# Kernel tuning notes

Hardware: AMD Instinct MI355X
Metric: run time of the kernel (lower is better)

The kernel has to match this reference:

```python
import jax, jax.numpy as jnp
import numpy as np

B, S, D, H, NL, V = 2, 512, 768, 12, 6, 32000
HD = D // H
EPS = 1e-6
# Faithful to original buffer: tril(ones, diagonal=-1) -> True strictly below diagonal,
# and masked_fill sets those to -inf (so each query attends to keys k >= q, as in the source).
MASK = jnp.tril(jnp.ones((S, S), dtype=bool), k=-1)


def setup_inputs() -> dict:
    key = jax.random.key(0)
    ks = jax.random.split(key, 12)
    sc = 0.02
    n = lambda k, shp: jax.random.normal(k, shp, dtype=jnp.float32) * sc
    return {
        "x": jax.random.randint(ks[0], (B, S), 0, V),
        "token_emb": n(ks[1], (V, D)),
        "pos_emb": n(ks[2], (S, D)),
        "norm1_s": jnp.ones((NL, D)), "norm1_b": jnp.zeros((NL, D)),
        "norm2_s": jnp.ones((NL, D)), "norm2_b": jnp.zeros((NL, D)),
        "wq": n(ks[3], (NL, D, D)), "wk": n(ks[4], (NL, D, D)), "wv": n(ks[5], (NL, D, D)),
        "wo": n(ks[6], (NL, D, D)), "bo": jnp.zeros((NL, D)),
        "w1": n(ks[7], (NL, D, 4 * D)), "b1": jnp.zeros((NL, 4 * D)),
        "w2": n(ks[8], (NL, 4 * D, D)), "b2": jnp.zeros((NL, D)),
        "final_s": jnp.ones((D,)), "final_b": jnp.zeros((D,)),
        "head_w": n(ks[9], (D, V)), "head_b": jnp.zeros((V,)),
    }


def _norm(x, s, b):
    # DummyNorm: torch.std default is unbiased (ddof=1); divides by (std + eps), no sqrt(var+eps)
    mean = x.mean(axis=-1, keepdims=True)
    std = jnp.std(x, axis=-1, ddof=1, keepdims=True)
    return s * (x - mean) / (std + EPS) + b


def _gelu(x):
    return 0.5 * x * (1.0 + jnp.tanh(jnp.sqrt(2.0 / jnp.pi) * (x + 0.044715 * x ** 3)))


def _block(x, p):
    wq, wk, wv, wo, bo, w1, b1, w2, b2, n1s, n1b, n2s, n2b = p
    res = x
    h = _norm(x, n1s, n1b)
    q = jnp.einsum("bsd,de->bse", h, wq).reshape(B, S, H, HD)
    k = jnp.einsum("bsd,de->bse", h, wk).reshape(B, S, H, HD)
    v = jnp.einsum("bsd,de->bse", h, wv).reshape(B, S, H, HD)
    scores = jnp.einsum("bqhd,bkhd->bhqk", q, k)
    scores = jnp.where(MASK, -jnp.inf, scores)
    w = jax.nn.softmax(scores / jnp.float32(HD) ** 0.5, axis=-1)  # dropout: eval mode (identity)
    ctx = jnp.einsum("bhqk,bkhd->bqhd", w, v).reshape(B, S, D)
    x = res + (ctx @ wo + bo)
    res = x
    h = _norm(x, n2s, n2b)
    x = res + (_gelu(h @ w1 + b1) @ w2 + b2)
    return x


def reference(x, token_emb, pos_emb, norm1_s, norm1_b, norm2_s, norm2_b,
              wq, wk, wv, wo, bo, w1, b1, w2, b2, final_s, final_b, head_w, head_b):
    h = token_emb[x] + pos_emb[None, :S, :]  # dropout is identity in eval
    params = (wq, wk, wv, wo, bo, w1, b1, w2, b2, norm1_s, norm1_b, norm2_s, norm2_b)
    h = jax.lax.scan(lambda c, p: (_block(c, p), None), h, params)[0]
    h = _norm(h, final_s, final_b)
    return h @ head_w + head_b  # [B, S, V]
```

## Files before the change

kernel.cpp:

```cpp
#include <hip/hip_runtime.h>
#include <math.h>

#define BDIM 2
#define SEQ 512
#define DMODEL 768
#define NHEAD 12
#define HDIM 64
#define NLAYER 6
#define VOCAB 32000
#define MROWS (BDIM*SEQ)
#define EPSV 1e-6f

typedef unsigned short u16;
typedef unsigned int u32;
typedef __bf16 bf16x8 __attribute__((ext_vector_type(8)));
typedef float f32x4 __attribute__((ext_vector_type(4)));

__device__ __forceinline__ u16 f2bf(float f) {
    union { float f; u32 u; } v; v.f = f;
    u32 r = v.u + 0x7fffu + ((v.u >> 16) & 1u);
    return (u16)(r >> 16);
}
__device__ __forceinline__ float bf2f(u16 b) {
    union { u32 u; float f; } v; v.u = ((u32)b) << 16;
    return v.f;
}

__device__ __forceinline__ void gload16(const u16* g, u16* l) {
    __builtin_amdgcn_global_load_lds(
        (const __attribute__((address_space(1))) unsigned int*)g,
        (__attribute__((address_space(3))) unsigned int*)l,
        16, 0, 0);
}

__global__ void embed_kernel(const int* __restrict__ x, const float* __restrict__ tok,
                             const float* __restrict__ pos, float* __restrict__ h) {
    int i = blockIdx.x * blockDim.x + threadIdx.x;
    if (i >= MROWS * DMODEL) return;
    int bs = i / DMODEL, d = i - bs * DMODEL;
    int s = bs & (SEQ - 1);
    h[i] = tok[(size_t)x[bs] * DMODEL + d] + pos[(size_t)s * DMODEL + d];
}

__global__ __launch_bounds__(256) void transpose_conv(const float* __restrict__ in, u16* __restrict__ out,
                                                      int K, int N, long in_bs, long out_bs) {
    __shared__ float t[64][65];
    int b = blockIdx.z;
    int n0 = blockIdx.x * 64, k0 = blockIdx.y * 64;
    int tid = threadIdx.x;
    const float* ip = in + (size_t)b * in_bs;
    int kr = tid >> 4, nc = (tid & 15) * 4;
    #pragma unroll
    for (int i = 0; i < 4; ++i) {
        float4 v = *(const float4*)(ip + (size_t)(k0 + kr + i * 16) * N + n0 + nc);
        t[kr + i * 16][nc] = v.x; t[kr + i * 16][nc + 1] = v.y;
        t[kr + i * 16][nc + 2] = v.z; t[kr + i * 16][nc + 3] = v.w;
    }
    __syncthreads();
    u16* op = out + (size_t)b * out_bs;
    int nr = tid >> 4, kc = (tid & 15) * 4;
    #pragma unroll
    for (int i = 0; i < 4; ++i) {
        ushort4 s;
        s.x = f2bf(t[kc + 0][nr + i * 16]);
        s.y = f2bf(t[kc + 1][nr + i * 16]);
        s.z = f2bf(t[kc + 2][nr + i * 16]);
        s.w = f2bf(t[kc + 3][nr + i * 16]);
        *(ushort4*)(op + (size_t)(n0 + nr + i * 16) * K + k0 + kc) = s;
    }
}

template<bool OUTBF>
__global__ __launch_bounds__(256) void norm_kernel(const float* __restrict__ in,
                                                   const float* __restrict__ scale,
                                                   const float* __restrict__ bias,
                                                   void* __restrict__ outp) {
    int row = blockIdx.x;
    const float* xr = in + (size_t)row * DMODEL;
    int t = threadIdx.x;
    float v0 = xr[t], v1 = xr[t + 256], v2 = xr[t + 512];

    float s = v0 + v1 + v2;
    for (int o = 32; o > 0; o >>= 1) s += __shfl_down(s, o);
    __shared__ float red1[4];
    __shared__ float red2[4];
    int wid = t >> 6, lane = t & 63;
    if (lane == 0) red1[wid] = s;
    __syncthreads();
    float mean = (red1[0] + red1[1] + red1[2] + red1[3]) * (1.0f / DMODEL);

    float d0 = v0 - mean, d1 = v1 - mean, d2 = v2 - mean;
    float ss = d0 * d0 + d1 * d1 + d2 * d2;
    for (int o = 32; o > 0; o >>= 1) ss += __shfl_xor(ss, o);
    if (lane == 0) red2[wid] = ss;
    __syncthreads();
    float var = (red2[0] + red2[1] + red2[2] + red2[3]) * (1.0f / (DMODEL - 1));
    float inv = 1.0f / (sqrtf(var) + EPSV);

    size_t o0 = (size_t)row * DMODEL + t;
    float r0 = scale[t] * d0 * inv + bias[t];
    float r1 = scale[t + 256] * d1 * inv + bias[t + 256];
    float r2 = scale[t + 512] * d2 * inv + bias[t + 512];
    if (OUTBF) {
        u16* out = (u16*)outp;
        out[o0] = f2bf(r0); out[o0 + 256] = f2bf(r1); out[o0 + 512] = f2bf(r2);
    } else {
        float* out = (float*)outp;
        out[o0] = r0; out[o0 + 256] = r1; out[o0 + 512] = r2;
    }
}


template<bool OUTBF, bool BIAS, bool RES, bool GELU, bool SWZ>
__global__ __launch_bounds__(256) void gemm_bf16(const u16* __restrict__ A,
                                                 const u16* __restrict__ Wt,
                                                 const float* __restrict__ bias,
                                                 const float* __restrict__ res,
                                                 void* __restrict__ Cout,
                                                 int M, int N, int K) {
    __shared__ u16 Alds[2][128 * 64];
    __shared__ u16 Blds[2][128 * 64];
    int tid = threadIdx.x;
    int lane = tid & 63;
    int wid = tid >> 6;
    int l15 = lane & 15, lk = lane >> 4;
    int wm = (wid >> 1) * 64, wn = (wid & 1) * 64;
    int bm, bn;
    if (SWZ) {
        int id = blockIdx.x;
        int xcd = id & 7, j = id >> 3;
        int g = xcd * ((int)gridDim.x >> 3) + j;
        int mb = M >> 7;
        bn = (g / mb) * 128;
        bm = (g % mb) * 128;
    } else {
        bm = blockIdx.y * 128; bn = blockIdx.x * 128;
    }

    f32x4 acc[4][4];
    #pragma unroll
    for (int i = 0; i < 4; ++i)
        #pragma unroll
        for (int j = 0; j < 4; ++j) { f32x4 z = {0.f, 0.f, 0.f, 0.f}; acc[i][j] = z; }

    int lr  = lane >> 3;
    int lc8 = (lane & 7) ^ lr;
    const u16* gA = A  + (size_t)(bm + lr) * K + lc8 * 8;
    const u16* gB = Wt + (size_t)(bn + lr) * K + lc8 * 8;
    int wrow = wid * 32;

    auto STAGE = [&](int buf, int k0) {
        #pragma unroll
        for (int i = 0; i < 4; ++i) {
            int rb = wrow + i * 8;
            gload16(gA + (size_t)rb * K + k0, &Alds[buf][rb * 64]);
            gload16(gB + (size_t)rb * K + k0, &Blds[buf][rb * 64]);
        }
    };

    STAGE(0, 0);
    __syncthreads();
    int nt = K >> 6;
    int cur = 0;
    for (int t = 0; t < nt; ++t) {
        if (t + 1 < nt) STAGE(cur ^ 1, (t + 1) << 6);

        #pragma unroll
        for (int s = 0; s < 2; ++s) {
            bf16x8 af[4], bfv[4];
            #pragma unroll
            for (int mi = 0; mi < 4; ++mi) {
                int R = wm + mi * 16 + l15;
                af[mi] = *(const bf16x8*)&Alds[cur][R * 64 + (((s * 4 + lk) ^ (R & 7)) << 3)];
            }
            #pragma unroll
            for (int ni = 0; ni < 4; ++ni) {
                int R = wn + ni * 16 + l15;
                bfv[ni] = *(const bf16x8*)&Blds[cur][R * 64 + (((s * 4 + lk) ^ (R & 7)) << 3)];
            }
            #pragma unroll
            for (int mi = 0; mi < 4; ++mi)
                #pragma unroll
                for (int ni = 0; ni < 4; ++ni)
                    acc[mi][ni] = __builtin_amdgcn_mfma_f32_16x16x32_bf16(af[mi], bfv[ni], acc[mi][ni], 0, 0, 0);
        }
        __syncthreads();
        cur ^= 1;
    }

    #pragma unroll
    for (int mi = 0; mi < 4; ++mi) {
        int row0 = bm + wm + mi * 16 + lk * 4;
        #pragma unroll
        for (int ni = 0; ni < 4; ++ni) {
            int col = bn + wn + ni * 16 + l15;
            float bv = BIAS ? bias[col] : 0.0f;
            #pragma unroll
            for (int rr = 0; rr < 4; ++rr) {
                int row = row0 + rr;
                float v = acc[mi][ni][rr] + bv;
                if (GELU) {
                    float xg = v;
                    v = 0.5f * xg * (1.0f + tanhf(0.7978845608028654f * (xg + 0.044715f * xg * xg * xg)));
                }
                if (RES) v += res[(size_t)row * N + col];
                if (OUTBF) ((u16*)Cout)[(size_t)row * N + col] = f2bf(v);
                else       ((float*)Cout)[(size_t)row * N + col] = v;
            }
        }
    }
}

template<bool OUTBF, bool BIAS, bool RES, bool GELU, int BM, int BN>
__global__ __launch_bounds__(256) void gemm_sm(const u16* __restrict__ A,
                                               const u16* __restrict__ Wt,
                                               const float* __restrict__ bias,
                                               const float* __restrict__ res,
                                               void* __restrict__ Cout,
                                               int M, int N, int K) {
    __shared__ u16 Alds[2][BM * 64];
    __shared__ u16 Blds[2][BN * 64];
    int tid = threadIdx.x;
    int lane = tid & 63;
    int wid = tid >> 6;
    int l15 = lane & 15, lk = lane >> 4;
    int wr = wid >> 1, wc = wid & 1;
    int id = blockIdx.x;
    int xcd = id & 7, j = id >> 3;
    int g = xcd * ((int)gridDim.x >> 3) + j;
    int mb = M / BM;
    int bn = (g / mb) * BN;
    int bm = (g % mb) * BM;
    constexpr int MI = BM / 32;
    constexpr int NI = BN / 32;

    f32x4 acc[MI][NI];
    #pragma unroll
    for (int i = 0; i < MI; ++i)
        #pragma unroll
        for (int j2 = 0; j2 < NI; ++j2) { f32x4 z = {0.f, 0.f, 0.f, 0.f}; acc[i][j2] = z; }

    int lr  = lane >> 3;
    int lc8 = (lane & 7) ^ lr;
    const u16* gA = A  + (size_t)(bm + lr) * K + lc8 * 8;
    const u16* gB = Wt + (size_t)(bn + lr) * K + lc8 * 8;

    auto STAGE = [&](int buf, int k0) {
        #pragma unroll
        for (int i = 0; i < MI; ++i) {
            int rb = wid * (BM / 4) + i * 8;
            gload16(gA + (size_t)rb * K + k0, &Alds[buf][rb * 64]);
        }
        #pragma unroll
        for (int i = 0; i < NI; ++i) {
            int rb = wid * (BN / 4) + i * 8;
            gload16(gB + (size_t)rb * K + k0, &Blds[buf][rb * 64]);
        }
    };

    STAGE(0, 0);
    __syncthreads();
    int nt = K >> 6;
    int cur = 0;
    for (int t = 0; t < nt; ++t) {
        if (t + 1 < nt) STAGE(cur ^ 1, (t + 1) << 6);

        #pragma unroll
        for (int s = 0; s < 2; ++s) {
            bf16x8 af[MI], bfv[NI];
            #pragma unroll
            for (int mi = 0; mi < MI; ++mi) {
                int R = wr * (BM / 2) + mi * 16 + l15;
                af[mi] = *(const bf16x8*)&Alds[cur][R * 64 + (((s * 4 + lk) ^ (R & 7)) << 3)];
            }
            #pragma unroll
            for (int ni = 0; ni < NI; ++ni) {
                int R = wc * (BN / 2) + ni * 16 + l15;
                bfv[ni] = *(const bf16x8*)&Blds[cur][R * 64 + (((s * 4 + lk) ^ (R & 7)) << 3)];
            }
            #pragma unroll
            for (int mi = 0; mi < MI; ++mi)
                #pragma unroll
                for (int ni = 0; ni < NI; ++ni)
                    acc[mi][ni] = __builtin_amdgcn_mfma_f32_16x16x32_bf16(af[mi], bfv[ni], acc[mi][ni], 0, 0, 0);
        }
        __syncthreads();
        cur ^= 1;
    }

    #pragma unroll
    for (int mi = 0; mi < MI; ++mi) {
        int row0 = bm + wr * (BM / 2) + mi * 16 + lk * 4;
        #pragma unroll
        for (int ni = 0; ni < NI; ++ni) {
            int col = bn + wc * (BN / 2) + ni * 16 + l15;
            float bv = BIAS ? bias[col] : 0.0f;
            #pragma unroll
            for (int rr = 0; rr < 4; ++rr) {
                int row = row0 + rr;
                float v = acc[mi][ni][rr] + bv;
                if (GELU) {
                    float xg = v;
                    v = 0.5f * xg * (1.0f + tanhf(0.7978845608028654f * (xg + 0.044715f * xg * xg * xg)));
                }
                if (RES) v += res[(size_t)row * N + col];
                if (OUTBF) ((u16*)Cout)[(size_t)row * N + col] = f2bf(v);
                else       ((float*)Cout)[(size_t)row * N + col] = v;
            }
        }
    }
}

__device__ __forceinline__ float bcast_q(float f0, float f1, float f2, float f3, int l15) {
    int src = (l15 >> 2) * 16;
    float a = __shfl(f0, src, 64);
    float b = __shfl(f1, src, 64);
    float c = __shfl(f2, src, 64);
    float d = __shfl(f3, src, 64);
    int r = l15 & 3;
    return r == 0 ? a : (r == 1 ? b : (r == 2 ? c : d));
}

__global__ __launch_bounds__(256) void attn_mfma(const u16* __restrict__ qkv, u16* __restrict__ ctx) {
    int id = blockIdx.x;
    int slot = id & 7, r0_ = id >> 3;
    int qt = r0_ & 7;
    int bh = (r0_ >> 3) * 8 + slot;
    int b = bh / NHEAD, h = bh % NHEAD;
    int tid = threadIdx.x;
    int w = tid >> 6, lane = tid & 63;
    int l15 = lane & 15, lk = lane >> 4;

    __shared__ u16 Klds[64][72];
    __shared__ u16 Vt[64][72];
    __shared__ u16 Plds[4][16][72];

    int q0 = qt * 64;
    const u16* qbase = qkv + (size_t)(b * SEQ + q0 + w * 16 + l15) * 2304 + h * HDIM;
    bf16x8 qf0 = *(const bf16x8*)(qbase + lk * 8);
    bf16x8 qf1 = *(const bf16x8*)(qbase + 32 + lk * 8);

    f32x4 acc_o[4];
    #pragma unroll
    for (int i = 0; i < 4; ++i) { f32x4 z = {0.f,0.f,0.f,0.f}; acc_o[i] = z; }
    float m_run[4] = {-INFINITY, -INFINITY, -INFINITY, -INFINITY};
    float l_run[4] = {0.f, 0.f, 0.f, 0.f};

    int srow = tid >> 2, sc = (tid & 3) * 16;
    int vcol = srow ^ ((sc >> 4) << 4);
    const u16* kg = qkv + (size_t)(b * SEQ) * 2304 + 768  + h * HDIM;
    const u16* vg = qkv + (size_t)(b * SEQ) * 2304 + 1536 + h * HDIM;

    for (int kt = qt; kt < SEQ / 64; ++kt) {
        int kk0 = kt * 64;
        const u16* kp = kg + (size_t)(kk0 + srow) * 2304 + sc;
        const u16* vp = vg + (size_t)(kk0 + srow) * 2304 + sc;
        uint4 kv0 = *(const uint4*)kp, kv1 = *(const uint4*)(kp + 8);
        uint4 vv0 = *(const uint4*)vp, vv1 = *(const uint4*)(vp + 8);
        __syncthreads();
        *(uint4*)&Klds[srow][sc]     = kv0;
        *(uint4*)&Klds[srow][sc + 8] = kv1;
        {
            const u16* vs = (const u16*)&vv0;
            #pragma unroll
            for (int i = 0; i < 8; ++i) Vt[sc + i][vcol] = vs[i];
            const u16* vs1 = (const u16*)&vv1;
            #pragma unroll
            for (int i = 0; i < 8; ++i) Vt[sc + 8 + i][vcol] = vs1[i];
        }
        __syncthreads();

        f32x4 accs[4];
        #pragma unroll
        for (int kb = 0; kb < 4; ++kb) { f32x4 z = {0.f,0.f,0.f,0.f}; accs[kb] = z; }
        __builtin_amdgcn_s_setprio(1);
        #pragma unroll
        for (int kb = 0; kb < 4; ++kb) {
            bf16x8 kf0 = *(const bf16x8*)&Klds[kb * 16 + l15][lk * 8];
            bf16x8 kf1 = *(const bf16x8*)&Klds[kb * 16 + l15][32 + lk * 8];
            accs[kb] = __builtin_amdgcn_mfma_f32_16x16x32_bf16(qf0, kf0, accs[kb], 0, 0, 0);
            accs[kb] = __builtin_amdgcn_mfma_f32_16x16x32_bf16(qf1, kf1, accs[kb], 0, 0, 0);
        }
        __builtin_amdgcn_s_setprio(0);

        bool diag = (kt == qt);
        float s[4][4];
        #pragma unroll
        for (int kb = 0; kb < 4; ++kb)
            #pragma unroll
            for (int r = 0; r < 4; ++r) {
                float v = accs[kb][r] * 0.125f;
                if (diag && (kk0 + kb * 16 + l15) < (q0 + w * 16 + lk * 4 + r)) v = -INFINITY;
                s[kb][r] = v;
            }
        float fac[4];
        #pragma unroll
        for (int r = 0; r < 4; ++r) {
            float mx = fmaxf(fmaxf(s[0][r], s[1][r]), fmaxf(s[2][r], s[3][r]));
            #pragma unroll
            for (int o = 8; o >= 1; o >>= 1) mx = fmaxf(mx, __shfl_xor(mx, o, 64));
            float mn = fmaxf(m_run[r], mx);
            fac[r] = expf(m_run[r] - mn);
            m_run[r] = mn;
        }
        u16 pb[4][4];
        #pragma unroll
        for (int r = 0; r < 4; ++r) {
            float rs = 0.f;
            #pragma unroll
            for (int kb = 0; kb < 4; ++kb) {
                float p = expf(s[kb][r] - m_run[r]);
                pb[kb][r] = f2bf(p);
                rs += p;
            }
            #pragma unroll
            for (int o = 8; o >= 1; o >>= 1) rs += __shfl_xor(rs, o, 64);
            l_run[r] = l_run[r] * fac[r] + rs;
        }
        #pragma unroll
        for (int kb = 0; kb < 4; ++kb)
            #pragma unroll
            for (int r = 0; r < 4; ++r)
                Plds[w][lk * 4 + r][kb * 16 + l15] = pb[kb][r];
        float fq = bcast_q(fac[0], fac[1], fac[2], fac[3], l15);
        #pragma unroll
        for (int db = 0; db < 4; ++db)
            #pragma unroll
            for (int r = 0; r < 4; ++r) acc_o[db][r] *= fq;
        __syncthreads();

        __builtin_amdgcn_s_setprio(1);
        #pragma unroll
        for (int ks = 0; ks < 2; ++ks) {
            bf16x8 pf = *(const bf16x8*)&Plds[w][l15][ks * 32 + lk * 8];
            #pragma unroll
            for (int db = 0; db < 4; ++db) {
                bf16x8 vf = *(const bf16x8*)&Vt[db * 16 + l15][(ks * 32 + lk * 8) ^ (db << 4)];
                acc_o[db] = __builtin_amdgcn_mfma_f32_16x16x32_bf16(vf, pf, acc_o[db], 0, 0, 0);
            }
        }
        __builtin_amdgcn_s_setprio(0);
    }

    float invq;
    {
        float i0 = 1.0f / l_run[0], i1 = 1.0f / l_run[1], i2 = 1.0f / l_run[2], i3 = 1.0f / l_run[3];
        invq = bcast_q(i0, i1, i2, i3, l15);
    }
    u16* cp = ctx + (size_t)(b * SEQ + q0 + w * 16 + l15) * DMODEL + h * HDIM;
    #pragma unroll
    for (int db = 0; db < 4; ++db) {
        ushort4 st;
        st.x = f2bf(acc_o[db][0] * invq);
        st.y = f2bf(acc_o[db][1] * invq);
        st.z = f2bf(acc_o[db][2] * invq);
        st.w = f2bf(acc_o[db][3] * invq);
        *(ushort4*)(cp + db * 16 + lk * 4) = st;
    }
}

template<bool BIAS, bool RES, bool GELU>
__global__ __launch_bounds__(256) void gemm_f32(const float* __restrict__ A, const float* __restrict__ W,
                                                const float* __restrict__ bias, const float* __restrict__ res,
                                                float* __restrict__ C, int M, int N, int K) {
    const int BM = 64, BN = 64, BK = 16;
    __shared__ float sA[BK][BM + 4];
    __shared__ float sB[BK][BN + 4];
    int tid = threadIdx.x;
    int tx = tid & 15, ty = tid >> 4;
    int bm = blockIdx.y * BM, bn = blockIdx.x * BN;
    float acc[4][4] = {};
    const float* Ab = A + (size_t)bm * K;
    const float* Wb = W + bn;
    for (int k0 = 0; k0 < K; k0 += BK) {
        {
            int rr = tid >> 2, c = (tid & 3) * 4;
            float4 va = *(const float4*)(Ab + (size_t)rr * K + k0 + c);
            sA[c + 0][rr] = va.x; sA[c + 1][rr] = va.y; sA[c + 2][rr] = va.z; sA[c + 3][rr] = va.w;
        }
        {
            int rr = tid >> 4, c = (tid & 15) * 4;
            float4 vb = *(const float4*)(Wb + (size_t)(k0 + rr) * N + c);
            *(float4*)(&sB[rr][c]) = vb;
        }
        __syncthreads();
        #pragma unroll
        for (int kk = 0; kk < BK; ++kk) {
            float4 a4 = *(const float4*)(&sA[kk][ty * 4]);
            float4 b4 = *(const float4*)(&sB[kk][tx * 4]);
            float a[4] = {a4.x, a4.y, a4.z, a4.w};
            float b[4] = {b4.x, b4.y, b4.z, b4.w};
            #pragma unroll
            for (int i = 0; i < 4; ++i)
                #pragma unroll
                for (int j = 0; j < 4; ++j) acc[i][j] += a[i] * b[j];
        }
        __syncthreads();
    }
    #pragma unroll
    for (int i = 0; i < 4; ++i) {
        int row = bm + ty * 4 + i;
        #pragma unroll
        for (int j = 0; j < 4; ++j) {
            int col = bn + tx * 4 + j;
            float v = acc[i][j];
            if (BIAS) v += bias[col];
            if (GELU) { float xg = v; v = 0.5f * xg * (1.0f + tanhf(0.7978845608028654f * (xg + 0.044715f * xg * xg * xg))); }
            if (RES) v += res[(size_t)row * N + col];
            C[(size_t)row * N + col] = v;
        }
    }
}

__global__ __launch_bounds__(256) void attn_f32(const float* __restrict__ q, const float* __restrict__ k,
                                                const float* __restrict__ v, float* __restrict__ ctx) {
    int blk = blockIdx.x;
    int qi = blk & (SEQ - 1);
    int tmp = blk >> 9;
    int h = tmp % NHEAD;
    int b = tmp / NHEAD;
    int tid = threadIdx.x;
    __shared__ float qv[HDIM];
    __shared__ float p[SEQ];
    __shared__ float rmax[4];
    __shared__ float rsum[4];
    __shared__ float part[4][HDIM];
    const float* qptr = q + ((size_t)(b * SEQ + qi) * DMODEL + h * HDIM);
    if (tid < HDIM) qv[tid] = qptr[tid];
    __syncthreads();
    float sc[2];
    #pragma unroll
    for (int c = 0; c < 2; ++c) {
        int kk = tid + c * 256;
        const float* kptr = k + ((size_t)(b * SEQ + kk) * DMODEL + h * HDIM);
        float dot = 0.0f;
        #pragma unroll
        for (int d = 0; d < HDIM; ++d) dot += qv[d] * kptr[d];
        sc[c] = (kk >= qi) ? dot * 0.125f : -INFINITY;
    }
    int wid = tid >> 6, lane = tid & 63;
    float m = fmaxf(sc[0], sc[1]);
    for (int o = 32; o > 0; o >>= 1) m = fmaxf(m, __shfl_down(m, o));
    if (lane == 0) rmax[wid] = m;
    __syncthreads();
    m = fmaxf(fmaxf(rmax[0], rmax[1]), fmaxf(rmax[2], rmax[3]));
    float e0 = expf(sc[0] - m);
    float e1 = expf(sc[1] - m);
    p[tid] = e0; p[tid + 256] = e1;
    float sum = e0 + e1;
    for (int o = 32; o > 0; o >>= 1) sum += __shfl_down(sum, o);
    if (lane == 0) rsum[wid] = sum;
    __syncthreads();
    float inv = 1.0f / (rsum[0] + rsum[1] + rsum[2] + rsum[3]);
    int d = tid & 63, ch = tid >> 6;
    float accv = 0.0f;
    const float* vbase = v + ((size_t)b * SEQ * DMODEL + h * HDIM + d);
    for (int kk = ch * 128; kk < (ch + 1) * 128; ++kk) accv += p[kk] * vbase[(size_t)kk * DMODEL];
    part[ch][d] = accv;
    __syncthreads();
    if (tid < HDIM) {
        float rv = (part[0][tid] + part[1][tid] + part[2][tid] + part[3][tid]) * inv;
        ctx[((size_t)(b * SEQ + qi) * DMODEL + h * HDIM + tid)] = rv;
    }
}

extern "C" void kernel_launch(void* const* d_in, const int* in_sizes, int n_in,
                              void* d_out, int out_size, void* d_ws, size_t ws_size,
                              hipStream_t stream) {
    const int*   x   = (const int*)d_in[0];
    const float* tok = (const float*)d_in[1];
    const float* pos = (const float*)d_in[2];
    const float* n1s = (const float*)d_in[3];
    const float* n1b = (const float*)d_in[4];
    const float* n2s = (const float*)d_in[5];
    const float* n2b = (const float*)d_in[6];
    const float* wq  = (const float*)d_in[7];
    const float* wk  = (const float*)d_in[8];
    const float* wv  = (const float*)d_in[9];
    const float* wo  = (const float*)d_in[10];
    const float* bo  = (const float*)d_in[11];
    const float* w1  = (const float*)d_in[12];
    const float* b1  = (const float*)d_in[13];
    const float* w2  = (const float*)d_in[14];
    const float* b2  = (const float*)d_in[15];
    const float* fs  = (const float*)d_in[16];
    const float* fb  = (const float*)d_in[17];
    const float* hw  = (const float*)d_in[18];
    const float* hb  = (const float*)d_in[19];
    float* out = (float*)d_out;

    const size_t szWtQKV = (size_t)NLAYER * 2304 * 768 * 2;
    const size_t szWtO   = (size_t)NLAYER * 768 * 768 * 2;
    const size_t szWt1   = (size_t)NLAYER * 3072 * 768 * 2;
    const size_t szWt2   = (size_t)NLAYER * 768 * 3072 * 2;
    const size_t szWtH   = (size_t)VOCAB * 768 * 2;
    const size_t szH     = (size_t)MROWS * DMODEL * 4;
    const size_t szHN    = (size_t)MROWS * DMODEL * 2;
    const size_t szQKV   = (size_t)MROWS * 2304 * 2;
    const size_t szCTX   = (size_t)MROWS * DMODEL * 2;
    const size_t szFF    = (size_t)MROWS * 3072 * 2;
    const size_t NEED = szWtQKV + szWtO + szWt1 + szWt2 + szWtH + szH + szHN + szQKV + szCTX + szFF;

    if (ws_size >= NEED) {
        char* p = (char*)d_ws;
        u16* WtQKV = (u16*)p; p += szWtQKV;
        u16* WtO   = (u16*)p; p += szWtO;
        u16* Wt1   = (u16*)p; p += szWt1;
        u16* Wt2   = (u16*)p; p += szWt2;
        u16* WtH   = (u16*)p; p += szWtH;
        float* h   = (float*)p; p += szH;
        u16* hn    = (u16*)p; p += szHN;
        u16* qkv   = (u16*)p; p += szQKV;
        u16* ctx   = (u16*)p; p += szCTX;
        u16* ff    = (u16*)p; p += szFF;

        transpose_conv<<<dim3(12, 12, NLAYER), 256, 0, stream>>>(wq, WtQKV + 0 * 768 * 768, 768, 768, 768 * 768, 2304 * 768);
        transpose_conv<<<dim3(12, 12, NLAYER), 256, 0, stream>>>(wk, WtQKV + 1 * 768 * 768, 768, 768, 768 * 768, 2304 * 768);
        transpose_conv<<<dim3(12, 12, NLAYER), 256, 0, stream>>>(wv, WtQKV + 2 * 768 * 768, 768, 768, 768 * 768, 2304 * 768);
        transpose_conv<<<dim3(12, 12, NLAYER), 256, 0, stream>>>(wo, WtO, 768, 768, 768 * 768, 768 * 768);
        transpose_conv<<<dim3(48, 12, NLAYER), 256, 0, stream>>>(w1, Wt1, 768, 3072, 768 * 3072, 3072 * 768);
        transpose_conv<<<dim3(12, 48, NLAYER), 256, 0, stream>>>(w2, Wt2, 3072, 768, 3072 * 768, 768 * 3072);
        transpose_conv<<<dim3(500, 12, 1), 256, 0, stream>>>(hw, WtH, 768, VOCAB, 0, 0);

        embed_kernel<<<(MROWS * DMODEL + 255) / 256, 256, 0, stream>>>(x, tok, pos, h);

        for (int l = 0; l < NLAYER; ++l) {
            const u16* wtqkv = WtQKV + (size_t)l * 2304 * 768;
            const u16* wto   = WtO   + (size_t)l * 768 * 768;
            const u16* wt1   = Wt1   + (size_t)l * 3072 * 768;
            const u16* wt2   = Wt2   + (size_t)l * 768 * 3072;

            norm_kernel<true><<<MROWS, 256, 0, stream>>>(h, n1s + l * DMODEL, n1b + l * DMODEL, hn);
            gemm_sm<true,false,false,false,64,64><<<576, 256, 0, stream>>>(hn, wtqkv, nullptr, nullptr, qkv, MROWS, 2304, 768);
            attn_mfma<<<192, 256, 0, stream>>>(qkv, ctx);
            gemm_sm<false,true,true,false,32,64><<<384, 256, 0, stream>>>(ctx, wto, bo + l * DMODEL, h, h, MROWS, 768, 768);
            norm_kernel<true><<<MROWS, 256, 0, stream>>>(h, n2s + l * DMODEL, n2b + l * DMODEL, hn);
            gemm_sm<true,true,false,true,64,64><<<768, 256, 0, stream>>>(hn, wt1, b1 + (size_t)l * 3072, nullptr, ff, MROWS, 3072, 768);
            gemm_sm<false,true,true,false,32,64><<<384, 256, 0, stream>>>(ff, wt2, b2 + l * DMODEL, h, h, MROWS, 768, 3072);
        }
        norm_kernel<true><<<MROWS, 256, 0, stream>>>(h, fs, fb, hn);
        gemm_bf16<false,true,false,false,true><<<2000, 256, 0, stream>>>(hn, WtH, hb, nullptr, out, MROWS, VOCAB, 768);
        return;
    }

    float* ws  = (float*)d_ws;
    float* h   = ws;
    float* hnf = h   + (size_t)MROWS * DMODEL;
    float* qb  = hnf + (size_t)MROWS * DMODEL;
    float* kb  = qb  + (size_t)MROWS * DMODEL;
    float* vb  = kb  + (size_t)MROWS * DMODEL;
    float* ctxf= vb  + (size_t)MROWS * DMODEL;
    float* fff = ctxf+ (size_t)MROWS * DMODEL;

    embed_kernel<<<(MROWS * DMODEL + 255) / 256, 256, 0, stream>>>(x, tok, pos, h);
    dim3 g768(DMODEL / 64, MROWS / 64);
    dim3 g3072(4 * DMODEL / 64, MROWS / 64);
    dim3 gV(VOCAB / 64, MROWS / 64);
    for (int l = 0; l < NLAYER; ++l) {
        size_t wOff  = (size_t)l * DMODEL * DMODEL;
        size_t w1Off = (size_t)l * DMODEL * 4 * DMODEL;
        norm_kernel<false><<<MROWS, 256, 0, stream>>>(h, n1s + l * DMODEL, n1b + l * DMODEL, hnf);
        gemm_f32<false,false,false><<<g768, 256, 0, stream>>>(hnf, wq + wOff, nullptr, nullptr, qb, MROWS, DMODEL, DMODEL);
        gemm_f32<false,false,false><<<g768, 256, 0, stream>>>(hnf, wk + wOff, nullptr, nullptr, kb, MROWS, DMODEL, DMODEL);
        gemm_f32<false,false,false><<<g768, 256, 0, stream>>>(hnf, wv + wOff, nullptr, nullptr, vb, MROWS, DMODEL, DMODEL);
        attn_f32<<<BDIM * NHEAD * SEQ, 256, 0, stream>>>(qb, kb, vb, ctxf);
        gemm_f32<true,true,false><<<g768, 256, 0, stream>>>(ctxf, wo + wOff, bo + l * DMODEL, h, h, MROWS, DMODEL, DMODEL);
        norm_kernel<false><<<MROWS, 256, 0, stream>>>(h, n2s + l * DMODEL, n2b + l * DMODEL, hnf);
        gemm_f32<true,false,true><<<g3072, 256, 0, stream>>>(hnf, w1 + w1Off, b1 + (size_t)l * 4 * DMODEL, nullptr, fff, MROWS, 4 * DMODEL, DMODEL);
        gemm_f32<true,true,false><<<g768, 256, 0, stream>>>(fff, w2 + w1Off, b2 + l * DMODEL, h, h, MROWS, DMODEL, 4 * DMODEL);
    }
    norm_kernel<false><<<MROWS, 256, 0, stream>>>(h, fs, fb, hnf);
    gemm_f32<true,false,false><<<gV, 256, 0, stream>>>(hnf, hw, hb, nullptr, out, MROWS, VOCAB, DMODEL);
}
```

Before: 798.0 us.

## Fuse layer norm into QKV and FFN1 GEMM prologue; merge QKVO transposes

Adds a GEMM kernel that computes per-row mean and unbiased std from the fp32 residual stream, then normalizes, converts to bf16 and writes A tiles into LDS on the fly. This removes the separate norm kernel launches and the bf16 normalized-activation round trip before the QKV and FFN1 GEMMs. The four Q/K/V/O weight transposes are also merged into one launch. In exchange, every N-block recomputes row statistics and re-reads fp32 activations plus scale and bias, so global read traffic and per-block work go up. The A loads become synchronous register loads instead of async copies.

```diff
diff --git a/kernel.cpp b/kernel.cpp
--- a/kernel.cpp
+++ b/kernel.cpp
@@ -67,6 +67,38 @@
         s.z = f2bf(t[kc + 2][nr + i * 16]);
         s.w = f2bf(t[kc + 3][nr + i * 16]);
         *(ushort4*)(op + (size_t)(n0 + nr + i * 16) * K + k0 + kc) = s;
+    }
+}
+
+__global__ __launch_bounds__(256) void transpose_qkvo(const float* __restrict__ wq, const float* __restrict__ wk,
+                                                      const float* __restrict__ wv, const float* __restrict__ wo,
+                                                      u16* __restrict__ WtQKV, u16* __restrict__ WtO) {
+    __shared__ float t[64][65];
+    int z = blockIdx.z;
+    int which = z & 3, l = z >> 2;
+    const float* srcs[4] = {wq, wk, wv, wo};
+    const float* ip = srcs[which] + (size_t)l * 768 * 768;
+    u16* op = (which < 3) ? (WtQKV + (size_t)l * 2304 * 768 + (size_t)which * 768 * 768)
+                          : (WtO + (size_t)l * 768 * 768);
+    int n0 = blockIdx.x * 64, k0 = blockIdx.y * 64;
+    int tid = threadIdx.x;
+    int kr = tid >> 4, nc = (tid & 15) * 4;
+    #pragma unroll
+    for (int i = 0; i < 4; ++i) {
+        float4 v = *(const float4*)(ip + (size_t)(k0 + kr + i * 16) * 768 + n0 + nc);
+        t[kr + i * 16][nc] = v.x; t[kr + i * 16][nc + 1] = v.y;
+        t[kr + i * 16][nc + 2] = v.z; t[kr + i * 16][nc + 3] = v.w;
+    }
+    __syncthreads();
+    int nr = tid >> 4, kc = (tid & 15) * 4;
+    #pragma unroll
+    for (int i = 0; i < 4; ++i) {
+        ushort4 s;
+        s.x = f2bf(t[kc + 0][nr + i * 16]);
+        s.y = f2bf(t[kc + 1][nr + i * 16]);
+        s.z = f2bf(t[kc + 2][nr + i * 16]);
+        s.w = f2bf(t[kc + 3][nr + i * 16]);
+        *(ushort4*)(op + (size_t)(n0 + nr + i * 16) * 768 + k0 + kc) = s;
     }
 }
 
@@ -311,6 +343,154 @@
     }
 }
 
+template<bool OUTBF, bool BIAS, bool GELU, int BN>
+__global__ __launch_bounds__(256) void gemm_nrm(const float* __restrict__ H,
+                                                const float* __restrict__ nsc,
+                                                const float* __restrict__ nbi,
+                                                const u16* __restrict__ Wt,
+                                                const float* __restrict__ bias,
+                                                void* __restrict__ Cout,
+                                                int M, int N, int K) {
+    constexpr int BM = 64;
+    __shared__ u16 Alds[2][BM * 64];
+    __shared__ u16 Blds[2][BN * 64];
+    __shared__ float smean[BM];
+    __shared__ float sinv[BM];
+    int tid = threadIdx.x;
+    int lane = tid & 63;
+    int wid = tid >> 6;
+    int l15 = lane & 15, lk = lane >> 4;
+    int wr = wid >> 1, wc = wid & 1;
+    int id = blockIdx.x;
+    int xcd = id & 7, j = id >> 3;
+    int g = xcd * ((int)gridDim.x >> 3) + j;
+    int mb = M / BM;
+    int bn = (g / mb) * BN;
+    int bm = (g % mb) * BM;
+    constexpr int NI = BN / 32;
+
+    for (int rr = 0; rr < 16; ++rr) {
+        int row = wid * 16 + rr;
+        const float* hr = H + (size_t)(bm + row) * K + lane * 4;
+        float4 a = *(const float4*)hr;
+        float4 b = *(const float4*)(hr + 256);
+        float4 c = *(const float4*)(hr + 512);
+        float s = a.x + a.y + a.z + a.w + b.x + b.y + b.z + b.w + c.x + c.y + c.z + c.w;
+        float q = a.x * a.x + a.y * a.y + a.z * a.z + a.w * a.w
+                + b.x * b.x + b.y * b.y + b.z * b.z + b.w * b.w
+                + c.x * c.x + c.y * c.y + c.z * c.z + c.w * c.w;
+        #pragma unroll
+        for (int o = 32; o > 0; o >>= 1) { s += __shfl_xor(s, o); q += __shfl_xor(q, o); }
+        if (lane == 0) {
+            float mean = s * (1.0f / 768.0f);
+            float var = (q - 768.0f * mean * mean) * (1.0f / 767.0f);
+            smean[row] = mean;
+            sinv[row] = 1.0f / (sqrtf(var) + EPSV);
+        }
+    }
+    __syncthreads();
+
+    int arow = tid >> 2;
+    int ac8  = (tid & 3) * 2;
+    const float* gH = H + (size_t)(bm + arow) * K;
+    float amean = smean[arow], ainv = sinv[arow];
+
+    int lr  = lane >> 3;
+    int lc8 = (lane & 7) ^ lr;
+    const u16* gB = Wt + (size_t)(bn + lr) * K + lc8 * 8;
+
+    auto STAGE_B = [&](int buf, int k0) {
+        #pragma unroll
+        for (int i = 0; i < NI; ++i) {
+            int rb = wid * (BN / 4) + i * 8;
+            gload16(gB + (size_t)rb * K + k0, &Blds[buf][rb * 64]);
+        }
+    };
+    auto STAGE_A = [&](int buf, int k0) {
+        #pragma unroll
+        for (int ch = 0; ch < 2; ++ch) {
+            int c8 = ac8 + ch;
+            int kb = k0 + c8 * 8;
+            float4 h0 = *(const float4*)(gH + kb);
+            float4 h1 = *(const float4*)(gH + kb + 4);
+            float4 s0 = *(const float4*)(nsc + kb);
+            float4 s1 = *(const float4*)(nsc + kb + 4);
+            float4 b0 = *(const float4*)(nbi + kb);
+            float4 b1 = *(const float4*)(nbi + kb + 4);
+            ushort4 o0, o1;
+            o0.x = f2bf(s0.x * (h0.x - amean) * ainv + b0.x);
+            o0.y = f2bf(s0.y * (h0.y - amean) * ainv + b0.y);
+            o0.z = f2bf(s0.z * (h0.z - amean) * ainv + b0.z);
+            o0.w = f2bf(s0.w * (h0.w - amean) * ainv + b0.w);
+            o1.x = f2bf(s1.x * (h1.x - amean) * ainv + b1.x);
+            o1.y = f2bf(s1.y * (h1.y - amean) * ainv + b1.y);
+            o1.z = f2bf(s1.z * (h1.z - amean) * ainv + b1.z);
+            o1.w = f2bf(s1.w * (h1.w - amean) * ainv + b1.w);
+            int dst = arow * 64 + ((c8 ^ (arow & 7)) << 3);
+            *(ushort4*)&Alds[buf][dst] = o0;
+            *(ushort4*)&Alds[buf][dst + 4] = o1;
+        }
+    };
+
+    f32x4 acc[2][NI];
+    #pragma unroll
+    for (int i = 0; i < 2; ++i)
+        #pragma unroll
+        for (int j2 = 0; j2 < NI; ++j2) { f32x4 z = {0.f, 0.f, 0.f, 0.f}; acc[i][j2] = z; }
+
+    STAGE_B(0, 0);
+    STAGE_A(0, 0);
+    __syncthreads();
+    int nt = K >> 6;
+    int cur = 0;
+    for (int t = 0; t < nt; ++t) {
+        if (t + 1 < nt) { STAGE_B(cur ^ 1, (t + 1) << 6); STAGE_A(cur ^ 1, (t + 1) << 6); }
+
+        #pragma unroll
+        for (int s = 0; s < 2; ++s) {
+            bf16x8 af[2], bfv[NI];
+            #pragma unroll
+            for (int mi = 0; mi < 2; ++mi) {
+                int R = wr * 32 + mi * 16 + l15;
+                af[mi] = *(const bf16x8*)&Alds[cur][R * 64 + (((s * 4 + lk) ^ (R & 7)) << 3)];
+            }
+            #pragma unroll
+            for (int ni = 0; ni < NI; ++ni) {
+                int R = wc * (BN / 2) + ni * 16 + l15;
+                bfv[ni] = *(const bf16x8*)&Blds[cur][R * 64 + (((s * 4 + lk) ^ (R & 7)) << 3)];
+            }
+            #pragma unroll
+            for (int mi = 0; mi < 2; ++mi)
+                #pragma unroll
+                for (int ni = 0; ni < NI; ++ni)
+                    acc[mi][ni] = __builtin_amdgcn_mfma_f32_16x16x32_bf16(af[mi], bfv[ni], acc[mi][ni], 0, 0, 0);
+        }
+        __syncthreads();
+        cur ^= 1;
+    }
+
+    #pragma unroll
+    for (int mi = 0; mi < 2; ++mi) {
+        int row0 = bm + wr * 32 + mi * 16 + lk * 4;
+        #pragma unroll
+        for (int ni = 0; ni < NI; ++ni) {
+            int col = bn + wc * (BN / 2) + ni * 16 + l15;
+            float bv = BIAS ? bias[col] : 0.0f;
+            #pragma unroll
+            for (int rr = 0; rr < 4; ++rr) {
+                int row = row0 + rr;
+                float v = acc[mi][ni][rr] + bv;
+                if (GELU) {
+                    float xg = v;
+                    v = 0.5f * xg * (1.0f + tanhf(0.7978845608028654f * (xg + 0.044715f * xg * xg * xg)));
+                }
+                if (OUTBF) ((u16*)Cout)[(size_t)row * N + col] = f2bf(v);
+                else       ((float*)Cout)[(size_t)row * N + col] = v;
+            }
+        }
+    }
+}
+
 __device__ __forceinline__ float bcast_q(float f0, float f1, float f2, float f3, int l15) {
     int src = (l15 >> 2) * 16;
     float a = __shfl(f0, src, 64);
@@ -614,10 +794,7 @@
         u16* ctx   = (u16*)p; p += szCTX;
         u16* ff    = (u16*)p; p += szFF;
 
-        transpose_conv<<<dim3(12, 12, NLAYER), 256, 0, stream>>>(wq, WtQKV + 0 * 768 * 768, 768, 768, 768 * 768, 2304 * 768);
-        transpose_conv<<<dim3(12, 12, NLAYER), 256, 0, stream>>>(wk, WtQKV + 1 * 768 * 768, 768, 768, 768 * 768, 2304 * 768);
-        transpose_conv<<<dim3(12, 12, NLAYER), 256, 0, stream>>>(wv, WtQKV + 2 * 768 * 768, 768, 768, 768 * 768, 2304 * 768);
-        transpose_conv<<<dim3(12, 12, NLAYER), 256, 0, stream>>>(wo, WtO, 768, 768, 768 * 768, 768 * 768);
+        transpose_qkvo<<<dim3(12, 12, 24), 256, 0, stream>>>(wq, wk, wv, wo, WtQKV, WtO);
         transpose_conv<<<dim3(48, 12, NLAYER), 256, 0, stream>>>(w1, Wt1, 768, 3072, 768 * 3072, 3072 * 768);
         transpose_conv<<<dim3(12, 48, NLAYER), 256, 0, stream>>>(w2, Wt2, 3072, 768, 3072 * 768, 768 * 3072);
         transpose_conv<<<dim3(500, 12, 1), 256, 0, stream>>>(hw, WtH, 768, VOCAB, 0, 0);
@@ -630,12 +807,10 @@
             const u16* wt1   = Wt1   + (size_t)l * 3072 * 768;
             const u16* wt2   = Wt2   + (size_t)l * 768 * 3072;
 
-            norm_kernel<true><<<MROWS, 256, 0, stream>>>(h, n1s + l * DMODEL, n1b + l * DMODEL, hn);
-            gemm_sm<true,false,false,false,64,64><<<576, 256, 0, stream>>>(hn, wtqkv, nullptr, nullptr, qkv, MROWS, 2304, 768);
+            gemm_nrm<true,false,false,64><<<576, 256, 0, stream>>>(h, n1s + l * DMODEL, n1b + l * DMODEL, wtqkv, nullptr, qkv, MROWS, 2304, 768);
             attn_mfma<<<192, 256, 0, stream>>>(qkv, ctx);
             gemm_sm<false,true,true,false,32,64><<<384, 256, 0, stream>>>(ctx, wto, bo + l * DMODEL, h, h, MROWS, 768, 768);
-            norm_kernel<true><<<MROWS, 256, 0, stream>>>(h, n2s + l * DMODEL, n2b + l * DMODEL, hn);
-            gemm_sm<true,true,false,true,64,64><<<768, 256, 0, stream>>>(hn, wt1, b1 + (size_t)l * 3072, nullptr, ff, MROWS, 3072, 768);
+            gemm_nrm<true,true,true,64><<<768, 256, 0, stream>>>(h, n2s + l * DMODEL, n2b + l * DMODEL, wt1, b1 + (size_t)l * 3072, ff, MROWS, 3072, 768);
             gemm_sm<false,true,true,false,32,64><<<384, 256, 0, stream>>>(ff, wt2, b2 + l * DMODEL, h, h, MROWS, 768, 3072);
         }
         norm_kernel<true><<<MROWS, 256, 0, stream>>>(h, fs, fb, hn);
```

After: 1.084 ms. +35.8%, slower.
